# Performance work log

Hardware: AMD Instinct MI355X
Metric: run time of the kernel (lower is better)

Reference implementation:

```python
import jax, jax.numpy as jnp
import numpy as np

V, E, H, B, S = 32000, 512, 1024, 128, 512
NEG = -1e9


def setup_inputs() -> dict:
    key = jax.random.key(0)
    ks = jax.random.split(key, 12)
    s = 0.02
    return {
        "previous_word": jax.random.randint(ks[0], (B, 1), 0, V),
        "h_0": jax.random.normal(ks[1], (B, H), jnp.float32),
        "c_0": jax.random.normal(ks[2], (B, H), jnp.float32),
        "ctx": jax.random.normal(ks[3], (B, S, H), jnp.float32),
        "ctx_mask": jnp.zeros((B, S), dtype=bool),
        "emb": jax.random.normal(ks[4], (V, E), jnp.float32) * s,
        "W_ih": jax.random.normal(ks[5], (4 * H, E), jnp.float32) * s,
        "W_hh": jax.random.normal(ks[6], (4 * H, H), jnp.float32) * s,
        "b_ih": jnp.zeros((4 * H,), jnp.float32),
        "b_hh": jnp.zeros((4 * H,), jnp.float32),
        "W_in": jax.random.normal(ks[7], (H, H), jnp.float32) * s,
        "W_out": jax.random.normal(ks[8], (H, 2 * H), jnp.float32) * s,
        "W_dec": jax.random.normal(ks[9], (V, H), jnp.float32) * s,
        "b_dec": jnp.zeros((V,), jnp.float32),
    }


def reference(previous_word, h_0, c_0, ctx, ctx_mask, emb, W_ih, W_hh, b_ih, b_hh, W_in, W_out, W_dec, b_dec):
    # embedding lookup + squeeze; dropout is identity in eval mode
    x = emb[previous_word[:, 0]]                       # [B, E]
    # LSTMCell: gate order i, f, g, o (PyTorch convention)
    gates = x @ W_ih.T + b_ih + h_0 @ W_hh.T + b_hh    # [B, 4H]
    i, f, g, o = jnp.split(gates, 4, axis=1)
    i = jax.nn.sigmoid(i)
    f = jax.nn.sigmoid(f)
    g = jnp.tanh(g)
    o = jax.nn.sigmoid(o)
    c_1 = f * c_0 + i * g
    h_1 = o * jnp.tanh(c_1)
    # SoftDotAttention
    target = h_1 @ W_in.T                               # [B, H]
    attn = jnp.einsum('bsh,bh->bs', ctx, target)        # [B, S]
    attn = jnp.where(ctx_mask, NEG, attn)
    alpha = jax.nn.softmax(attn, axis=1)
    weighted = jnp.einsum('bs,bsh->bh', alpha, ctx)     # [B, H]
    h_tilde = jnp.tanh(jnp.concatenate([weighted, h_1], axis=1) @ W_out.T)
    logit = h_tilde @ W_dec.T + b_dec                   # [B, V]
    return (h_1, c_1, alpha, logit)
```

## Files before the change

kernel.cpp:

```cpp
#include <hip/hip_runtime.h>
#include <hip/hip_bf16.h>
#include <cstdint>

#define NEG_BIG (-1.0e9f)

typedef __attribute__((ext_vector_type(8))) short short8_t;
typedef __attribute__((ext_vector_type(4))) float f32x4;

typedef __attribute__((address_space(1))) const unsigned int gu32_t;
typedef __attribute__((address_space(3))) unsigned int lu32_t;

__device__ __forceinline__ short f2bf(float x) {
  union { float f; unsigned u; } v; v.f = x;
  unsigned r = v.u + 0x7fffu + ((v.u >> 16) & 1u);
  return (short)(r >> 16);
}
__device__ __forceinline__ float sigmoidf_(float x) { return 1.0f / (1.0f + __expf(-x)); }

__device__ __forceinline__ void block_barrier() {
  asm volatile("" ::: "memory");
  __builtin_amdgcn_s_barrier();
  asm volatile("" ::: "memory");
}

__global__ void k_pack_a1(const int* __restrict__ prev, const float* __restrict__ emb,
                          const float* __restrict__ h0, short* __restrict__ A1) {
  int t = blockIdx.x * 256 + threadIdx.x;
  if (t >= 128 * 1536) return;
  int b = t / 1536, k = t - b * 1536;
  float v = (k < 512) ? emb[(size_t)prev[b] * 512 + k] : h0[b * 1024 + (k - 512)];
  A1[t] = f2bf(v);
}

template <int MB, int WN, int EPI>
__launch_bounds__(256, 2)
__global__ void k_gemm(const short* __restrict__ A, int lda,
                       const float* __restrict__ Wa, int ldwa, int Ka,
                       const float* __restrict__ Wb, int ldwb, int Ktot,
                       const float* __restrict__ bias0, const float* __restrict__ bias1,
                       float* __restrict__ outF, short* __restrict__ outB, int ldo) {
  constexpr int BN = WN * 16;
  constexpr int MREP = (MB == 128) ? 2 * WN : 1;
  constexpr int AU = MB / 32;
  constexpr int WLOADS = (BN * 64) / 1024;
  __shared__ __align__(16) short lA[2][MB * 64];
  __shared__ __align__(16) short lW[2][BN * 64];
  const int tid = threadIdx.x;
  const int wid = tid >> 6, l = tid & 63, l15 = l & 15, khalf = l >> 4;
  const int nblk = blockIdx.x;
  const int mrow0 = blockIdx.y * MB;
  const int m_wave = (WN == 1) ? wid * (MB / 4) : 0;
  const int nb_local = (WN == 4) ? wid * 16 : 0;

  const int arow = (MB == 128) ? (tid >> 1) : (tid >> 2);
  const int apart = (MB == 128) ? (tid & 1) : (tid & 3);
  const int abase = apart * (AU * 16);
  const int aswz = (arow & 7) << 4;
  const short* Arow = A + (size_t)(mrow0 + arow) * lda + apart * (AU * 8);

  int wn_[WLOADS], wkq_[WLOADS];
#pragma unroll
  for (int j = 0; j < WLOADS; ++j) {
    int idx = j * 1024 + tid * 4;
    wn_[j] = idx >> 6;
    wkq_[j] = idx & 63;
  }

  f32x4 acc[MREP];
#pragma unroll
  for (int r = 0; r < MREP; ++r) acc[r] = (f32x4){0.f, 0.f, 0.f, 0.f};

  short8_t aR[AU];
  float4 wR[WLOADS];

  auto stage_regs = [&](int k0) {
#pragma unroll
    for (int q = 0; q < AU; ++q) aR[q] = *(const short8_t*)(Arow + k0 + q * 8);
#pragma unroll
    for (int j = 0; j < WLOADS; ++j) {
      int kg = k0 + wkq_[j];
      const float* p = (kg < Ka) ? (Wa + (size_t)(nblk * BN + wn_[j]) * ldwa + kg)
                                 : (Wb + (size_t)(nblk * BN + wn_[j]) * ldwb + (kg - Ka));
      wR[j] = *(const float4*)p;
    }
  };
  auto write_lds = [&](int buf) {
    char* drow = (char*)lA[buf] + arow * 128;
#pragma unroll
    for (int q = 0; q < AU; ++q)
      *(short8_t*)(drow + ((abase + q * 16) ^ aswz)) = aR[q];
#pragma unroll
    for (int j = 0; j < WLOADS; ++j) {
      short4 h4;
      h4.x = f2bf(wR[j].x); h4.y = f2bf(wR[j].y); h4.z = f2bf(wR[j].z); h4.w = f2bf(wR[j].w);
      *(short4*)((char*)lW[buf] + wn_[j] * 128 + ((wkq_[j] * 2) ^ ((wn_[j] & 7) << 4))) = h4;
    }
  };
  auto compute = [&](int buf) {
#pragma unroll
    for (int ks = 0; ks < 2; ++ks) {
      const int ubyte = ks * 64 + khalf * 16;
      const int nrow = nb_local + l15;
      short8_t bfrag = *(const short8_t*)((char*)lW[buf] + nrow * 128 + (ubyte ^ ((nrow & 7) << 4)));
#pragma unroll
      for (int r = 0; r < MREP; ++r) {
        const int mrow = m_wave + r * 16 + l15;
        short8_t afrag = *(const short8_t*)((char*)lA[buf] + mrow * 128 + (ubyte ^ ((mrow & 7) << 4)));
        acc[r] = __builtin_amdgcn_mfma_f32_16x16x32_bf16(afrag, bfrag, acc[r], 0, 0, 0);
      }
    }
  };

  const int NT = Ktot >> 6;
  stage_regs(0);
  write_lds(0);
  for (int t = 0; t < NT; ++t) {
    const int cur = t & 1;
    if (t + 1 < NT) stage_regs((t + 1) << 6);
    __syncthreads();
    compute(cur);
    if (t + 1 < NT) write_lds(cur ^ 1);
  }

  const int n = nblk * BN + nb_local + l15;
  float bias = 0.f;
  if (bias0) bias = bias0[n];
  if (bias1) bias += bias1[n];
#pragma unroll
  for (int r = 0; r < MREP; ++r) {
    int mb = mrow0 + m_wave + r * 16 + khalf * 4;
#pragma unroll
    for (int e = 0; e < 4; ++e) {
      float v = acc[r][e] + bias;
      if (EPI == 1) {
        outB[(size_t)(mb + e) * ldo + n] = f2bf(tanhf(v));
      } else {
        outF[(size_t)(mb + e) * ldo + n] = v;
      }
    }
  }
}

__global__ void k_lstm(const float* __restrict__ gates, const float* __restrict__ c0,
                       float* __restrict__ h1_out, float* __restrict__ c1_out,
                       short* __restrict__ A3) {
  int t = blockIdx.x * 256 + threadIdx.x;
  int b = t >> 10, h = t & 1023;
  const float* g = gates + (size_t)b * 4096;
  float ig = sigmoidf_(g[h]);
  float fg = sigmoidf_(g[1024 + h]);
  float gg = tanhf(g[2048 + h]);
  float og = sigmoidf_(g[3072 + h]);
  float c1 = fg * c0[t] + ig * gg;
  float h1 = og * tanhf(c1);
  c1_out[t] = c1;
  h1_out[t] = h1;
  A3[(size_t)b * 2048 + 1024 + h] = f2bf(h1);
}

__launch_bounds__(256, 2)
__global__ void k_attn(const float* __restrict__ ctx, const float* __restrict__ target,
                       const unsigned char* __restrict__ mask,
                       float* __restrict__ scores, float* __restrict__ part) {
  __shared__ __align__(16) float lds[2][8 * 1024];
  const int b = blockIdx.x >> 3, chunk = blockIdx.x & 7;
  const int tid = threadIdx.x;
  const int wid = tid >> 6, l = tid & 63;
  const float* tg = target + (size_t)b * 1024;
  float4 t4[4], w4[4];
#pragma unroll
  for (int j = 0; j < 4; ++j) {
    t4[j] = *(const float4*)(tg + j * 256 + l * 4);
    w4[j].x = 0.f; w4[j].y = 0.f; w4[j].z = 0.f; w4[j].w = 0.f;
  }
  float m = -INFINITY, lsum = 0.f;
  const int s0 = chunk * 64;
  const float* cb = ctx + ((size_t)b * 512 + s0) * 1024;
  const unsigned char* mk = mask + (size_t)b * 512 + s0;

  auto stage = [&](int buf, int tt) {
    const char* src = (const char*)(cb + (size_t)tt * 8192);
    char* dst = (char*)&lds[buf][0];
#pragma unroll
    for (int i = 0; i < 8; ++i) {
      const int off = i * 4096 + tid * 16;
      __builtin_amdgcn_global_load_lds((gu32_t*)(src + off), (lu32_t*)(dst + off), 16, 0, 0);
    }
  };

  stage(0, 0);
  int buf = 0;
  for (int t = 0; t < 8; ++t) {
    if (t < 7) {
      stage(buf ^ 1, t + 1);
      asm volatile("s_waitcnt vmcnt(8)" ::: "memory");
    } else {
      asm volatile("s_waitcnt vmcnt(0)" ::: "memory");
    }
    block_barrier();
#pragma unroll
    for (int rr = 0; rr < 2; ++rr) {
      const int r = wid * 2 + rr;
      const float* row = &lds[buf][r * 1024];
      float4 c0 = *(const float4*)(row + l * 4);
      float4 c1 = *(const float4*)(row + 256 + l * 4);
      float4 c2 = *(const float4*)(row + 512 + l * 4);
      float4 c3 = *(const float4*)(row + 768 + l * 4);
      float p = c0.x * t4[0].x + c0.y * t4[0].y + c0.z * t4[0].z + c0.w * t4[0].w +
                c1.x * t4[1].x + c1.y * t4[1].y + c1.z * t4[1].z + c1.w * t4[1].w +
                c2.x * t4[2].x + c2.y * t4[2].y + c2.z * t4[2].z + c2.w * t4[2].w +
                c3.x * t4[3].x + c3.y * t4[3].y + c3.z * t4[3].z + c3.w * t4[3].w;
#pragma unroll
      for (int off = 32; off > 0; off >>= 1) p += __shfl_xor(p, off);
      const int sg = t * 8 + r;
      if (mk[sg]) p = NEG_BIG;
      if (l == 0) scores[(size_t)b * 512 + s0 + sg] = p;
      float mn = fmaxf(m, p);
      float scale = __expf(m - mn);
      float e = __expf(p - mn);
      lsum = lsum * scale + e;
      w4[0].x = w4[0].x * scale + e * c0.x; w4[0].y = w4[0].y * scale + e * c0.y;
      w4[0].z = w4[0].z * scale + e * c0.z; w4[0].w = w4[0].w * scale + e * c0.w;
      w4[1].x = w4[1].x * scale + e * c1.x; w4[1].y = w4[1].y * scale + e * c1.y;
      w4[1].z = w4[1].z * scale + e * c1.z; w4[1].w = w4[1].w * scale + e * c1.w;
      w4[2].x = w4[2].x * scale + e * c2.x; w4[2].y = w4[2].y * scale + e * c2.y;
      w4[2].z = w4[2].z * scale + e * c2.z; w4[2].w = w4[2].w * scale + e * c2.w;
      w4[3].x = w4[3].x * scale + e * c3.x; w4[3].y = w4[3].y * scale + e * c3.y;
      w4[3].z = w4[3].z * scale + e * c3.z; w4[3].w = w4[3].w * scale + e * c3.w;
      m = mn;
    }
    block_barrier();
    buf ^= 1;
  }
  float* pp = part + ((size_t)b * 32 + (chunk * 4 + wid)) * 1028;
#pragma unroll
  for (int j = 0; j < 4; ++j) *(float4*)(pp + j * 256 + l * 4) = w4[j];
  if (l == 0) { pp[1024] = m; pp[1025] = lsum; }
}

__launch_bounds__(256, 4)
__global__ void k_finish(const float* __restrict__ scores, const float* __restrict__ part,
                         float* __restrict__ alpha, short* __restrict__ A3) {
  __shared__ float sm[32], sl[32];
  int b = blockIdx.x, t = threadIdx.x;
  if (t < 32) {
    sm[t] = part[((size_t)b * 32 + t) * 1028 + 1024];
    sl[t] = part[((size_t)b * 32 + t) * 1028 + 1025];
  }
  __syncthreads();
  float M = -INFINITY;
#pragma unroll
  for (int i = 0; i < 32; ++i) M = fmaxf(M, sm[i]);
  float scl[32];
  float L = 0.f;
#pragma unroll
  for (int i = 0; i < 32; ++i) {
    scl[i] = __expf(sm[i] - M);
    L += sl[i] * scl[i];
  }
  float inv = 1.0f / L;
  float s0 = scores[(size_t)b * 512 + t];
  float s1 = scores[(size_t)b * 512 + 256 + t];
  alpha[(size_t)b * 512 + t] = __expf(s0 - M) * inv;
  alpha[(size_t)b * 512 + 256 + t] = __expf(s1 - M) * inv;
  float ax = 0.f, ay = 0.f, az = 0.f, aw = 0.f;
#pragma unroll
  for (int i = 0; i < 32; ++i) {
    const float4 w = *(const float4*)(part + ((size_t)b * 32 + i) * 1028 + t * 4);
    ax += scl[i] * w.x; ay += scl[i] * w.y; az += scl[i] * w.z; aw += scl[i] * w.w;
  }
  short4 o4;
  o4.x = f2bf(ax * inv); o4.y = f2bf(ay * inv); o4.z = f2bf(az * inv); o4.w = f2bf(aw * inv);
  *(short4*)(A3 + (size_t)b * 2048 + t * 4) = o4;
}

extern "C" void kernel_launch(void* const* d_in, const int* in_sizes, int n_in,
                              void* d_out, int out_size, void* d_ws, size_t ws_size,
                              hipStream_t stream) {
  const int* prev = (const int*)d_in[0];
  const float* h0 = (const float*)d_in[1];
  const float* c0 = (const float*)d_in[2];
  const float* ctx = (const float*)d_in[3];
  const unsigned char* mask = (const unsigned char*)d_in[4];
  const float* emb = (const float*)d_in[5];
  const float* W_ih = (const float*)d_in[6];
  const float* W_hh = (const float*)d_in[7];
  const float* b_ih = (const float*)d_in[8];
  const float* b_hh = (const float*)d_in[9];
  const float* W_in = (const float*)d_in[10];
  const float* W_out = (const float*)d_in[11];
  const float* W_dec = (const float*)d_in[12];
  const float* b_dec = (const float*)d_in[13];

  float* out_h1 = (float*)d_out;
  float* out_c1 = out_h1 + 128 * 1024;
  float* out_alpha = out_c1 + 128 * 1024;
  float* out_logit = out_alpha + 128 * 512;

  char* ws = (char*)d_ws;
  short* A1 = (short*)(ws + 0x000000);
  float* gates = (float*)(ws + 0x060000);
  short* A3 = (short*)(ws + 0x260000);
  float* target = (float*)(ws + 0x2E0000);
  float* scores = (float*)(ws + 0x360000);
  float* part = (float*)(ws + 0x3A0000);
  short* htilde = (short*)(ws + 0x1400000);

  k_pack_a1<<<768, 256, 0, stream>>>(prev, emb, h0, A1);
  k_gemm<128, 1, 0><<<dim3(256, 1), 256, 0, stream>>>(A1, 1536, W_ih, 512, 512, W_hh, 1024,
                                                      1536, b_ih, b_hh, gates, nullptr, 4096);
  k_lstm<<<512, 256, 0, stream>>>(gates, c0, out_h1, out_c1, A3);
  k_gemm<64, 1, 0><<<dim3(64, 2), 256, 0, stream>>>(A3 + 1024, 2048, W_in, 1024, 1024, W_in,
                                                    1024, 1024, nullptr, nullptr, target,
                                                    nullptr, 1024);
  k_attn<<<1024, 256, 0, stream>>>(ctx, target, mask, scores, part);
  k_finish<<<128, 256, 0, stream>>>(scores, part, out_alpha, A3);
  k_gemm<64, 1, 1><<<dim3(64, 2), 256, 0, stream>>>(A3, 2048, W_out, 2048, 2048, W_out, 2048,
                                                    2048, nullptr, nullptr, nullptr, htilde,
                                                    1024);
  k_gemm<128, 4, 0><<<dim3(500, 1), 256, 0, stream>>>(htilde, 1024, W_dec, 1024, 1024, W_dec,
                                                      1024, 1024, b_dec, nullptr, out_logit,
                                                      nullptr, 32000);
}
```

Measured before the change: 158.7 us.

## Fuse embedding gather, gate GEMM and LSTM cell; halve attention split count

Replaces the pack, gate-GEMM and LSTM pointwise kernels with one kernel. It gathers embedding and h0 rows directly, does the bf16 MFMA over both weight matrices with gate-interleaved column tiles, and applies the LSTM cell in the epilogue through LDS. This removes two launches and the round trips of the packed A1 and fp32 gates buffers through global memory. Attention now uses 4 chunks of 128 positions per batch instead of 8, so there are fewer partials to merge, at the cost of half as many blocks. The GEMM barriers are also replaced with an explicit lgkmcnt wait plus s_barrier.

```diff
diff --git a/kernel.cpp b/kernel.cpp
--- a/kernel.cpp
+++ b/kernel.cpp
@@ -17,19 +17,135 @@
 }
 __device__ __forceinline__ float sigmoidf_(float x) { return 1.0f / (1.0f + __expf(-x)); }
 
+__device__ __forceinline__ void lds_barrier() {
+  asm volatile("s_waitcnt lgkmcnt(0)\n\ts_barrier" ::: "memory");
+}
 __device__ __forceinline__ void block_barrier() {
   asm volatile("" ::: "memory");
   __builtin_amdgcn_s_barrier();
   asm volatile("" ::: "memory");
 }
 
-__global__ void k_pack_a1(const int* __restrict__ prev, const float* __restrict__ emb,
-                          const float* __restrict__ h0, short* __restrict__ A1) {
-  int t = blockIdx.x * 256 + threadIdx.x;
-  if (t >= 128 * 1536) return;
-  int b = t / 1536, k = t - b * 1536;
-  float v = (k < 512) ? emb[(size_t)prev[b] * 512 + k] : h0[b * 1024 + (k - 512)];
-  A1[t] = f2bf(v);
+__launch_bounds__(256, 2)
+__global__ void k_gates(const int* __restrict__ prev, const float* __restrict__ emb,
+                        const float* __restrict__ h0,
+                        const float* __restrict__ W_ih, const float* __restrict__ W_hh,
+                        const float* __restrict__ b_ih, const float* __restrict__ b_hh,
+                        const float* __restrict__ c0,
+                        float* __restrict__ h1_out, float* __restrict__ c1_out,
+                        short* __restrict__ A3) {
+  __shared__ __align__(16) short lA[2][64 * 64];
+  __shared__ __align__(16) short lW[2][64 * 64];
+  const int tid = threadIdx.x;
+  const int wid = tid >> 6, l = tid & 63, l15 = l & 15, khalf = l >> 4;
+  const int hb = blockIdx.x;
+  const int mrow0 = blockIdx.y * 64;
+
+  const int arow = tid >> 2;
+  const int apart = tid & 3;
+  const int aswz = (arow & 7) << 4;
+  const int bA = mrow0 + arow;
+  const int pv = prev[bA];
+  const float* embrow = emb + (size_t)pv * 512 + apart * 16;
+  const float* h0row = h0 + (size_t)bA * 1024 + apart * 16;
+
+  int wrow_[4], wkq_[4];
+  const float* wih_[4];
+  const float* whh_[4];
+#pragma unroll
+  for (int j = 0; j < 4; ++j) {
+    int idx = j * 1024 + tid * 4;
+    int n = idx >> 6;
+    wkq_[j] = idx & 63;
+    wrow_[j] = n;
+    int grow = (n >> 4) * 1024 + hb * 16 + (n & 15);
+    wih_[j] = W_ih + (size_t)grow * 512;
+    whh_[j] = W_hh + (size_t)grow * 1024;
+  }
+
+  f32x4 acc[4];
+#pragma unroll
+  for (int r = 0; r < 4; ++r) acc[r] = (f32x4){0.f, 0.f, 0.f, 0.f};
+
+  float4 aF[4], wR[4];
+  auto stage_regs = [&](int k0) {
+    const float* asrc = (k0 < 512) ? (embrow + k0) : (h0row + (k0 - 512));
+#pragma unroll
+    for (int q = 0; q < 4; ++q) aF[q] = *(const float4*)(asrc + q * 4);
+#pragma unroll
+    for (int j = 0; j < 4; ++j) {
+      int kg = k0 + wkq_[j];
+      wR[j] = (kg < 512) ? *(const float4*)(wih_[j] + kg)
+                         : *(const float4*)(whh_[j] + (kg - 512));
+    }
+  };
+  auto write_lds = [&](int buf) {
+    char* drow = (char*)lA[buf] + arow * 128;
+#pragma unroll
+    for (int q = 0; q < 2; ++q) {
+      short8_t s;
+      s[0] = f2bf(aF[2 * q].x); s[1] = f2bf(aF[2 * q].y);
+      s[2] = f2bf(aF[2 * q].z); s[3] = f2bf(aF[2 * q].w);
+      s[4] = f2bf(aF[2 * q + 1].x); s[5] = f2bf(aF[2 * q + 1].y);
+      s[6] = f2bf(aF[2 * q + 1].z); s[7] = f2bf(aF[2 * q + 1].w);
+      *(short8_t*)(drow + ((apart * 32 + q * 16) ^ aswz)) = s;
+    }
+#pragma unroll
+    for (int j = 0; j < 4; ++j) {
+      short4 h4;
+      h4.x = f2bf(wR[j].x); h4.y = f2bf(wR[j].y); h4.z = f2bf(wR[j].z); h4.w = f2bf(wR[j].w);
+      *(short4*)((char*)lW[buf] + wrow_[j] * 128 + ((wkq_[j] * 2) ^ ((wrow_[j] & 7) << 4))) = h4;
+    }
+  };
+  auto compute = [&](int buf) {
+#pragma unroll
+    for (int ks = 0; ks < 2; ++ks) {
+      const int ubyte = ks * 64 + khalf * 16;
+      const int nrow = wid * 16 + l15;
+      short8_t bfrag = *(const short8_t*)((char*)lW[buf] + nrow * 128 + (ubyte ^ ((nrow & 7) << 4)));
+#pragma unroll
+      for (int r = 0; r < 4; ++r) {
+        const int mrow = r * 16 + l15;
+        short8_t afrag = *(const short8_t*)((char*)lA[buf] + mrow * 128 + (ubyte ^ ((mrow & 7) << 4)));
+        acc[r] = __builtin_amdgcn_mfma_f32_16x16x32_bf16(afrag, bfrag, acc[r], 0, 0, 0);
+      }
+    }
+  };
+
+  stage_regs(0);
+  write_lds(0);
+  for (int t = 0; t < 24; ++t) {
+    const int cur = t & 1;
+    if (t + 1 < 24) stage_regs((t + 1) << 6);
+    lds_barrier();
+    compute(cur);
+    if (t + 1 < 24) write_lds(cur ^ 1);
+  }
+
+  lds_barrier();
+  float* gbuf = (float*)&lA[0][0];
+#pragma unroll
+  for (int r = 0; r < 4; ++r)
+#pragma unroll
+    for (int e = 0; e < 4; ++e)
+      gbuf[wid * 1024 + (r * 16 + khalf * 4 + e) * 16 + l15] = acc[r][e];
+  __syncthreads();
+#pragma unroll
+  for (int q = 0; q < 4; ++q) {
+    int idx = q * 256 + tid;
+    int hloc = idx & 15, mloc = idx >> 4;
+    int b = mrow0 + mloc;
+    int hh = hb * 16 + hloc;
+    float iv = gbuf[0 + mloc * 16 + hloc] + b_ih[hh] + b_hh[hh];
+    float fv = gbuf[1024 + mloc * 16 + hloc] + b_ih[1024 + hh] + b_hh[1024 + hh];
+    float gv = gbuf[2048 + mloc * 16 + hloc] + b_ih[2048 + hh] + b_hh[2048 + hh];
+    float ov = gbuf[3072 + mloc * 16 + hloc] + b_ih[3072 + hh] + b_hh[3072 + hh];
+    float c1 = sigmoidf_(fv) * c0[(size_t)b * 1024 + hh] + sigmoidf_(iv) * tanhf(gv);
+    float h1 = sigmoidf_(ov) * tanhf(c1);
+    c1_out[(size_t)b * 1024 + hh] = c1;
+    h1_out[(size_t)b * 1024 + hh] = h1;
+    A3[(size_t)b * 2048 + 1024 + hh] = f2bf(h1);
+  }
 }
 
 template <int MB, int WN, int EPI>
@@ -117,7 +233,7 @@
   for (int t = 0; t < NT; ++t) {
     const int cur = t & 1;
     if (t + 1 < NT) stage_regs((t + 1) << 6);
-    __syncthreads();
+    lds_barrier();
     compute(cur);
     if (t + 1 < NT) write_lds(cur ^ 1);
   }
@@ -141,29 +257,12 @@
   }
 }
 
-__global__ void k_lstm(const float* __restrict__ gates, const float* __restrict__ c0,
-                       float* __restrict__ h1_out, float* __restrict__ c1_out,
-                       short* __restrict__ A3) {
-  int t = blockIdx.x * 256 + threadIdx.x;
-  int b = t >> 10, h = t & 1023;
-  const float* g = gates + (size_t)b * 4096;
-  float ig = sigmoidf_(g[h]);
-  float fg = sigmoidf_(g[1024 + h]);
-  float gg = tanhf(g[2048 + h]);
-  float og = sigmoidf_(g[3072 + h]);
-  float c1 = fg * c0[t] + ig * gg;
-  float h1 = og * tanhf(c1);
-  c1_out[t] = c1;
-  h1_out[t] = h1;
-  A3[(size_t)b * 2048 + 1024 + h] = f2bf(h1);
-}
-
 __launch_bounds__(256, 2)
 __global__ void k_attn(const float* __restrict__ ctx, const float* __restrict__ target,
                        const unsigned char* __restrict__ mask,
                        float* __restrict__ scores, float* __restrict__ part) {
   __shared__ __align__(16) float lds[2][8 * 1024];
-  const int b = blockIdx.x >> 3, chunk = blockIdx.x & 7;
+  const int b = blockIdx.x >> 2, chunk = blockIdx.x & 3;
   const int tid = threadIdx.x;
   const int wid = tid >> 6, l = tid & 63;
   const float* tg = target + (size_t)b * 1024;
@@ -174,7 +273,7 @@
     w4[j].x = 0.f; w4[j].y = 0.f; w4[j].z = 0.f; w4[j].w = 0.f;
   }
   float m = -INFINITY, lsum = 0.f;
-  const int s0 = chunk * 64;
+  const int s0 = chunk * 128;
   const float* cb = ctx + ((size_t)b * 512 + s0) * 1024;
   const unsigned char* mk = mask + (size_t)b * 512 + s0;
 
@@ -190,8 +289,8 @@
 
   stage(0, 0);
   int buf = 0;
-  for (int t = 0; t < 8; ++t) {
-    if (t < 7) {
+  for (int t = 0; t < 16; ++t) {
+    if (t < 15) {
       stage(buf ^ 1, t + 1);
       asm volatile("s_waitcnt vmcnt(8)" ::: "memory");
     } else {
@@ -232,7 +331,7 @@
     block_barrier();
     buf ^= 1;
   }
-  float* pp = part + ((size_t)b * 32 + (chunk * 4 + wid)) * 1028;
+  float* pp = part + ((size_t)b * 16 + (chunk * 4 + wid)) * 1028;
 #pragma unroll
   for (int j = 0; j < 4; ++j) *(float4*)(pp + j * 256 + l * 4) = w4[j];
   if (l == 0) { pp[1024] = m; pp[1025] = lsum; }
@@ -241,20 +340,20 @@
 __launch_bounds__(256, 4)
 __global__ void k_finish(const float* __restrict__ scores, const float* __restrict__ part,
                          float* __restrict__ alpha, short* __restrict__ A3) {
-  __shared__ float sm[32], sl[32];
+  __shared__ float sm[16], sl[16];
   int b = blockIdx.x, t = threadIdx.x;
-  if (t < 32) {
-    sm[t] = part[((size_t)b * 32 + t) * 1028 + 1024];
-    sl[t] = part[((size_t)b * 32 + t) * 1028 + 1025];
+  if (t < 16) {
+    sm[t] = part[((size_t)b * 16 + t) * 1028 + 1024];
+    sl[t] = part[((size_t)b * 16 + t) * 1028 + 1025];
   }
   __syncthreads();
   float M = -INFINITY;
 #pragma unroll
-  for (int i = 0; i < 32; ++i) M = fmaxf(M, sm[i]);
-  float scl[32];
+  for (int i = 0; i < 16; ++i) M = fmaxf(M, sm[i]);
+  float scl[16];
   float L = 0.f;
 #pragma unroll
-  for (int i = 0; i < 32; ++i) {
+  for (int i = 0; i < 16; ++i) {
     scl[i] = __expf(sm[i] - M);
     L += sl[i] * scl[i];
   }
@@ -265,8 +364,8 @@
   alpha[(size_t)b * 512 + 256 + t] = __expf(s1 - M) * inv;
   float ax = 0.f, ay = 0.f, az = 0.f, aw = 0.f;
 #pragma unroll
-  for (int i = 0; i < 32; ++i) {
-    const float4 w = *(const float4*)(part + ((size_t)b * 32 + i) * 1028 + t * 4);
+  for (int i = 0; i < 16; ++i) {
+    const float4 w = *(const float4*)(part + ((size_t)b * 16 + i) * 1028 + t * 4);
     ax += scl[i] * w.x; ay += scl[i] * w.y; az += scl[i] * w.z; aw += scl[i] * w.w;
   }
   short4 o4;
@@ -298,22 +397,18 @@
   float* out_logit = out_alpha + 128 * 512;
 
   char* ws = (char*)d_ws;
-  short* A1 = (short*)(ws + 0x000000);
-  float* gates = (float*)(ws + 0x060000);
-  short* A3 = (short*)(ws + 0x260000);
-  float* target = (float*)(ws + 0x2E0000);
-  float* scores = (float*)(ws + 0x360000);
-  float* part = (float*)(ws + 0x3A0000);
-  short* htilde = (short*)(ws + 0x1400000);
-
-  k_pack_a1<<<768, 256, 0, stream>>>(prev, emb, h0, A1);
-  k_gemm<128, 1, 0><<<dim3(256, 1), 256, 0, stream>>>(A1, 1536, W_ih, 512, 512, W_hh, 1024,
-                                                      1536, b_ih, b_hh, gates, nullptr, 4096);
-  k_lstm<<<512, 256, 0, stream>>>(gates, c0, out_h1, out_c1, A3);
+  short* A3 = (short*)(ws + 0x000000);
+  float* target = (float*)(ws + 0x100000);
+  float* scores = (float*)(ws + 0x200000);
+  float* part = (float*)(ws + 0x300000);
+  short* htilde = (short*)(ws + 0xD00000);
+
+  k_gates<<<dim3(64, 2), 256, 0, stream>>>(prev, emb, h0, W_ih, W_hh, b_ih, b_hh, c0,
+                                           out_h1, out_c1, A3);
   k_gemm<64, 1, 0><<<dim3(64, 2), 256, 0, stream>>>(A3 + 1024, 2048, W_in, 1024, 1024, W_in,
                                                     1024, 1024, nullptr, nullptr, target,
                                                     nullptr, 1024);
-  k_attn<<<1024, 256, 0, stream>>>(ctx, target, mask, scores, part);
+  k_attn<<<512, 256, 0, stream>>>(ctx, target, mask, scores, part);
   k_finish<<<128, 256, 0, stream>>>(scores, part, out_alpha, A3);
   k_gemm<64, 1, 1><<<dim3(64, 2), 256, 0, stream>>>(A3, 2048, W_out, 2048, 2048, W_out, 2048,
                                                     2048, nullptr, nullptr, nullptr, htilde,
```

After: 149.2 us. 1.06x faster.

## Split-K the small target and output GEMMs, halve attention blocks

Applied to the files above, without the earlier changes.

Adds split-K support to the GEMM kernel through a blockIdx.z offset. The W_in GEMM now runs with 4 K-slices and the W_out GEMM with 8 K-slices, writing partial sums. The attention kernel sums the four target partials on load, and a new k_htilde kernel sums the eight output partials and applies tanh. Attention now processes 128 sequence rows per block over 512 blocks, and finish merges 16 partials instead of 32. The GEMM loop barrier is replaced by an inline-asm lgkmcnt wait plus s_barrier. This aims to fill the GPU for the small-M GEMMs, at the cost of an extra launch, extra partial-sum memory traffic and fewer attention blocks.

```diff
diff --git a/kernel.cpp b/kernel.cpp
--- a/kernel.cpp
+++ b/kernel.cpp
@@ -17,6 +17,9 @@
 }
 __device__ __forceinline__ float sigmoidf_(float x) { return 1.0f / (1.0f + __expf(-x)); }
 
+__device__ __forceinline__ void lds_barrier() {
+  asm volatile("s_waitcnt lgkmcnt(0)\n\ts_barrier" ::: "memory");
+}
 __device__ __forceinline__ void block_barrier() {
   asm volatile("" ::: "memory");
   __builtin_amdgcn_s_barrier();
@@ -38,13 +41,18 @@
                        const float* __restrict__ Wa, int ldwa, int Ka,
                        const float* __restrict__ Wb, int ldwb, int Ktot,
                        const float* __restrict__ bias0, const float* __restrict__ bias1,
-                       float* __restrict__ outF, short* __restrict__ outB, int ldo) {
+                       float* __restrict__ outF, short* __restrict__ outB, int ldo,
+                       int kstride, size_t pstride) {
   constexpr int BN = WN * 16;
   constexpr int MREP = (MB == 128) ? 2 * WN : 1;
   constexpr int AU = MB / 32;
   constexpr int WLOADS = (BN * 64) / 1024;
   __shared__ __align__(16) short lA[2][MB * 64];
   __shared__ __align__(16) short lW[2][BN * 64];
+  const int kc = blockIdx.z;
+  A += (size_t)kc * kstride;
+  Wa += (size_t)kc * kstride;
+  if (outF) outF += (size_t)kc * pstride;
   const int tid = threadIdx.x;
   const int wid = tid >> 6, l = tid & 63, l15 = l & 15, khalf = l >> 4;
   const int nblk = blockIdx.x;
@@ -117,7 +125,7 @@
   for (int t = 0; t < NT; ++t) {
     const int cur = t & 1;
     if (t + 1 < NT) stage_regs((t + 1) << 6);
-    __syncthreads();
+    lds_barrier();
     compute(cur);
     if (t + 1 < NT) write_lds(cur ^ 1);
   }
@@ -159,22 +167,27 @@
 }
 
 __launch_bounds__(256, 2)
-__global__ void k_attn(const float* __restrict__ ctx, const float* __restrict__ target,
+__global__ void k_attn(const float* __restrict__ ctx, const float* __restrict__ tp,
                        const unsigned char* __restrict__ mask,
                        float* __restrict__ scores, float* __restrict__ part) {
   __shared__ __align__(16) float lds[2][8 * 1024];
-  const int b = blockIdx.x >> 3, chunk = blockIdx.x & 7;
+  const int b = blockIdx.x >> 2, chunk = blockIdx.x & 3;
   const int tid = threadIdx.x;
   const int wid = tid >> 6, l = tid & 63;
-  const float* tg = target + (size_t)b * 1024;
   float4 t4[4], w4[4];
 #pragma unroll
   for (int j = 0; j < 4; ++j) {
-    t4[j] = *(const float4*)(tg + j * 256 + l * 4);
+    float4 a = {0.f, 0.f, 0.f, 0.f};
+#pragma unroll
+    for (int p = 0; p < 4; ++p) {
+      const float4 v = *(const float4*)(tp + (size_t)p * 131072 + (size_t)b * 1024 + j * 256 + l * 4);
+      a.x += v.x; a.y += v.y; a.z += v.z; a.w += v.w;
+    }
+    t4[j] = a;
     w4[j].x = 0.f; w4[j].y = 0.f; w4[j].z = 0.f; w4[j].w = 0.f;
   }
   float m = -INFINITY, lsum = 0.f;
-  const int s0 = chunk * 64;
+  const int s0 = chunk * 128;
   const float* cb = ctx + ((size_t)b * 512 + s0) * 1024;
   const unsigned char* mk = mask + (size_t)b * 512 + s0;
 
@@ -190,8 +203,8 @@
 
   stage(0, 0);
   int buf = 0;
-  for (int t = 0; t < 8; ++t) {
-    if (t < 7) {
+  for (int t = 0; t < 16; ++t) {
+    if (t < 15) {
       stage(buf ^ 1, t + 1);
       asm volatile("s_waitcnt vmcnt(8)" ::: "memory");
     } else {
@@ -232,7 +245,7 @@
     block_barrier();
     buf ^= 1;
   }
-  float* pp = part + ((size_t)b * 32 + (chunk * 4 + wid)) * 1028;
+  float* pp = part + ((size_t)b * 16 + (chunk * 4 + wid)) * 1028;
 #pragma unroll
   for (int j = 0; j < 4; ++j) *(float4*)(pp + j * 256 + l * 4) = w4[j];
   if (l == 0) { pp[1024] = m; pp[1025] = lsum; }
@@ -241,20 +254,20 @@
 __launch_bounds__(256, 4)
 __global__ void k_finish(const float* __restrict__ scores, const float* __restrict__ part,
                          float* __restrict__ alpha, short* __restrict__ A3) {
-  __shared__ float sm[32], sl[32];
+  __shared__ float sm[16], sl[16];
   int b = blockIdx.x, t = threadIdx.x;
-  if (t < 32) {
-    sm[t] = part[((size_t)b * 32 + t) * 1028 + 1024];
-    sl[t] = part[((size_t)b * 32 + t) * 1028 + 1025];
+  if (t < 16) {
+    sm[t] = part[((size_t)b * 16 + t) * 1028 + 1024];
+    sl[t] = part[((size_t)b * 16 + t) * 1028 + 1025];
   }
   __syncthreads();
   float M = -INFINITY;
 #pragma unroll
-  for (int i = 0; i < 32; ++i) M = fmaxf(M, sm[i]);
-  float scl[32];
+  for (int i = 0; i < 16; ++i) M = fmaxf(M, sm[i]);
+  float scl[16];
   float L = 0.f;
 #pragma unroll
-  for (int i = 0; i < 32; ++i) {
+  for (int i = 0; i < 16; ++i) {
     scl[i] = __expf(sm[i] - M);
     L += sl[i] * scl[i];
   }
@@ -265,13 +278,21 @@
   alpha[(size_t)b * 512 + 256 + t] = __expf(s1 - M) * inv;
   float ax = 0.f, ay = 0.f, az = 0.f, aw = 0.f;
 #pragma unroll
-  for (int i = 0; i < 32; ++i) {
-    const float4 w = *(const float4*)(part + ((size_t)b * 32 + i) * 1028 + t * 4);
+  for (int i = 0; i < 16; ++i) {
+    const float4 w = *(const float4*)(part + ((size_t)b * 16 + i) * 1028 + t * 4);
     ax += scl[i] * w.x; ay += scl[i] * w.y; az += scl[i] * w.z; aw += scl[i] * w.w;
   }
   short4 o4;
   o4.x = f2bf(ax * inv); o4.y = f2bf(ay * inv); o4.z = f2bf(az * inv); o4.w = f2bf(aw * inv);
   *(short4*)(A3 + (size_t)b * 2048 + t * 4) = o4;
+}
+
+__global__ void k_htilde(const float* __restrict__ wp, short* __restrict__ ht) {
+  int t = blockIdx.x * 256 + threadIdx.x;
+  float s = 0.f;
+#pragma unroll
+  for (int p = 0; p < 8; ++p) s += wp[(size_t)p * 131072 + t];
+  ht[t] = f2bf(tanhf(s));
 }
 
 extern "C" void kernel_launch(void* const* d_in, const int* in_sizes, int n_in,
@@ -298,27 +319,29 @@
   float* out_logit = out_alpha + 128 * 512;
 
   char* ws = (char*)d_ws;
-  short* A1 = (short*)(ws + 0x000000);
-  float* gates = (float*)(ws + 0x060000);
-  short* A3 = (short*)(ws + 0x260000);
-  float* target = (float*)(ws + 0x2E0000);
-  float* scores = (float*)(ws + 0x360000);
-  float* part = (float*)(ws + 0x3A0000);
+  short* A3 = (short*)(ws + 0x000000);
+  float* scores = (float*)(ws + 0x100000);
+  float* tp = (float*)(ws + 0x200000);
+  float* part = (float*)(ws + 0x400000);
+  float* wp = (float*)(ws + 0xD00000);
+  float* gates = (float*)(ws + 0x1100000);
+  short* A1 = (short*)(ws + 0x1300000);
   short* htilde = (short*)(ws + 0x1400000);
 
   k_pack_a1<<<768, 256, 0, stream>>>(prev, emb, h0, A1);
-  k_gemm<128, 1, 0><<<dim3(256, 1), 256, 0, stream>>>(A1, 1536, W_ih, 512, 512, W_hh, 1024,
-                                                      1536, b_ih, b_hh, gates, nullptr, 4096);
+  k_gemm<128, 1, 0><<<dim3(256, 1, 1), 256, 0, stream>>>(
+      A1, 1536, W_ih, 512, 512, W_hh, 1024, 1536, b_ih, b_hh, gates, nullptr, 4096, 0, 0);
   k_lstm<<<512, 256, 0, stream>>>(gates, c0, out_h1, out_c1, A3);
-  k_gemm<64, 1, 0><<<dim3(64, 2), 256, 0, stream>>>(A3 + 1024, 2048, W_in, 1024, 1024, W_in,
-                                                    1024, 1024, nullptr, nullptr, target,
-                                                    nullptr, 1024);
-  k_attn<<<1024, 256, 0, stream>>>(ctx, target, mask, scores, part);
+  k_gemm<128, 1, 0><<<dim3(64, 1, 4), 256, 0, stream>>>(
+      A3 + 1024, 2048, W_in, 1024, 1 << 30, W_in, 1024, 256, nullptr, nullptr, tp, nullptr,
+      1024, 256, (size_t)131072);
+  k_attn<<<512, 256, 0, stream>>>(ctx, tp, mask, scores, part);
   k_finish<<<128, 256, 0, stream>>>(scores, part, out_alpha, A3);
-  k_gemm<64, 1, 1><<<dim3(64, 2), 256, 0, stream>>>(A3, 2048, W_out, 2048, 2048, W_out, 2048,
-                                                    2048, nullptr, nullptr, nullptr, htilde,
-                                                    1024);
-  k_gemm<128, 4, 0><<<dim3(500, 1), 256, 0, stream>>>(htilde, 1024, W_dec, 1024, 1024, W_dec,
-                                                      1024, 1024, b_dec, nullptr, out_logit,
-                                                      nullptr, 32000);
-}
+  k_gemm<128, 1, 0><<<dim3(64, 1, 8), 256, 0, stream>>>(
+      A3, 2048, W_out, 2048, 1 << 30, W_out, 2048, 256, nullptr, nullptr, wp, nullptr,
+      1024, 256, (size_t)131072);
+  k_htilde<<<512, 256, 0, stream>>>(wp, htilde);
+  k_gemm<128, 4, 0><<<dim3(500, 1, 1), 256, 0, stream>>>(
+      htilde, 1024, W_dec, 1024, 1024, W_dec, 1024, 1024, b_dec, nullptr, out_logit, nullptr,
+      32000, 0, 0);
+}
```

Measured after the change: 134.3 us, median of 3. 15.4% less time.
